# Performance work log

Measured on AMD Instinct MI355X. Metric: run time of the kernel, lower is better.

## Reference

```python
import jax, jax.numpy as jnp
import numpy as np

B, S, D_MODEL, HEADS, DK = 2, 2048, 1024, 16, 64


def setup_inputs() -> dict:
    key = jax.random.key(0)
    ks = jax.random.split(key, 7)
    scale = 0.02
    return {
        "query": jax.random.normal(ks[0], (B, S, D_MODEL), jnp.float32),
        "key": jax.random.normal(ks[1], (B, S, D_MODEL), jnp.float32),
        "value": jax.random.normal(ks[2], (B, S, D_MODEL), jnp.float32),
        "Wq": jax.random.normal(ks[3], (D_MODEL, HEADS * DK), jnp.float32) * scale,
        "bq": jax.random.normal(ks[4], (HEADS * DK,), jnp.float32) * scale,
        "Wo": jax.random.normal(ks[5], (HEADS * DK, D_MODEL), jnp.float32) * scale,
        "bo": jax.random.normal(ks[6], (D_MODEL,), jnp.float32) * scale,
    }


def reference(query, key, value, Wq, bq, Wo, bo):
    # NOTE: faithful to the original code, which (buggily) uses _W_q to
    # project query, key AND value, and scales by sqrt(seq_len), not sqrt(d_k).
    seq_len = key.shape[1]

    def split_heads(x):
        # [B,S,H*DK] -> [H,B,S,DK]; torch chunk(dim=-1)+cat(dim=0) stacks head h
        # (slice h*DK:(h+1)*DK) at batch block h.
        p = x @ Wq + bq
        b, s, _ = p.shape
        return p.reshape(b, s, HEADS, DK).transpose(2, 0, 1, 3)

    q = split_heads(query)   # [H,B,S,DK]
    k = split_heads(key)
    v = split_heads(value)

    inv_scale = jnp.float32(1.0 / np.sqrt(seq_len))
    scores = jnp.einsum("hbqd,hbkd->hbqk", q, k) * inv_scale  # [H,B,S,S]
    attn = jax.nn.softmax(scores, axis=-1)
    out = jnp.einsum("hbqk,hbkd->hbqd", attn, v)  # [H,B,S,DK]
    # inverse of chunk(dim=0)+cat(dim=-1): [H,B,S,DK] -> [B,S,H*DK]
    out = out.transpose(1, 2, 0, 3).reshape(query.shape[0], query.shape[1], HEADS * DK)
    return out @ Wo + bo
```

## Files before the change

kernel.cpp:

```cpp
#include <hip/hip_runtime.h>

#define DEVI __device__ __forceinline__

typedef short short4_t __attribute__((ext_vector_type(4)));
typedef short short8_t __attribute__((ext_vector_type(8)));
typedef __bf16 bf16x8 __attribute__((ext_vector_type(8)));
typedef float f32x4 __attribute__((ext_vector_type(4)));

DEVI short f2bf(float f) {
    union { float f; unsigned u; } v; v.f = f;
    unsigned r = (v.u + 0x7fffu + ((v.u >> 16) & 1u)) >> 16;
    return (short)r;
}

DEVI unsigned pack_ru(float a, float b) {
    union { float f; unsigned u; } x, y; x.f = a; y.f = b;
    return __builtin_amdgcn_perm(y.u + 0x8000u, x.u + 0x8000u, 0x07060302u);
}

DEVI void g2lds16(const short* g, short* l) {
    __builtin_amdgcn_global_load_lds(
        (const __attribute__((address_space(1))) void*)g,
        (__attribute__((address_space(3))) void*)l, 16, 0, 0);
}

__global__ __launch_bounds__(256) void cvt3_kernel(const float* __restrict__ q,
                                                   const float* __restrict__ k,
                                                   const float* __restrict__ v,
                                                   short* __restrict__ X) {
    const size_t N1 = (size_t)4096 * 1024;
    size_t e = ((size_t)blockIdx.x * 256 + threadIdx.x) * 4;
    const float* src; size_t off;
    if (e < N1)            { src = q; off = e; }
    else if (e < 2 * N1)   { src = k; off = e - N1; }
    else                   { src = v; off = e - 2 * N1; }
    f32x4 f = *(const f32x4*)(src + off);
    short4_t o;
    o[0] = f2bf(f[0]); o[1] = f2bf(f[1]); o[2] = f2bf(f[2]); o[3] = f2bf(f[3]);
    *(short4_t*)(X + e) = o;
}

__global__ __launch_bounds__(256) void transpose_w_kernel(const float* __restrict__ W,
                                                          short* __restrict__ Wt) {
    __shared__ short T[64][65];
    const int t = threadIdx.x;
    const int kt = blockIdx.x * 64, nt = blockIdx.y * 64;
#pragma unroll
    for (int r = 0; r < 4; ++r) {
        int kl = (t >> 4) + 16 * r;
        int n0 = (t & 15) * 4;
        f32x4 f = *(const f32x4*)(W + (size_t)(kt + kl) * 1024 + nt + n0);
#pragma unroll
        for (int j = 0; j < 4; ++j) T[n0 + j][kl] = f2bf(f[j]);
    }
    __syncthreads();
#pragma unroll
    for (int r = 0; r < 2; ++r) {
        int nl = (t >> 3) + 32 * r;
        int k0 = (t & 7) * 8;
        short8_t v;
#pragma unroll
        for (int j = 0; j < 8; ++j) v[j] = T[nl][k0 + j];
        *(short8_t*)(Wt + (size_t)(nt + nl) * 1024 + kt + k0) = v;
    }
}

template <typename OutT>
__global__ __launch_bounds__(256) void gemm_bt_kernel(const short* __restrict__ A,
                                                      const short* __restrict__ Bt,
                                                      const float* __restrict__ bias,
                                                      OutT* __restrict__ C,
                                                      int M, int N, int K,
                                                      int qrows, float qscale) {
    __shared__ __align__(16) short As[128 * 32];
    __shared__ __align__(16) short Bs[128 * 32];
    const int tid  = threadIdx.x;
    const int lane = tid & 63, wave = tid >> 6;
    const int quad = lane >> 4, l16 = lane & 15;
    const int row0 = blockIdx.x * 128, col0 = blockIdx.y * 128;
    const int wm = (wave >> 1) * 64, wn = (wave & 1) * 64;
    const int srow = lane >> 2;
    const int scol = (lane & 3) * 8;
    f32x4 acc[4][4] = {};
    for (int k0 = 0; k0 < K; k0 += 32) {
#pragma unroll
        for (int r = 0; r < 2; ++r) {
            int rb = r * 64 + wave * 16;
            g2lds16(A  + (size_t)(row0 + rb + srow) * K + k0 + scol, &As[rb * 32]);
            g2lds16(Bt + (size_t)(col0 + rb + srow) * K + k0 + scol, &Bs[rb * 32]);
        }
        __syncthreads();
        bf16x8 af[4], bfr[4];
#pragma unroll
        for (int mi = 0; mi < 4; ++mi) af[mi]  = *(const bf16x8*)&As[(wm + mi * 16 + l16) * 32 + quad * 8];
#pragma unroll
        for (int ni = 0; ni < 4; ++ni) bfr[ni] = *(const bf16x8*)&Bs[(wn + ni * 16 + l16) * 32 + quad * 8];
#pragma unroll
        for (int mi = 0; mi < 4; ++mi)
#pragma unroll
            for (int ni = 0; ni < 4; ++ni)
                acc[mi][ni] = __builtin_amdgcn_mfma_f32_16x16x32_bf16(af[mi], bfr[ni], acc[mi][ni], 0, 0, 0);
        __syncthreads();
    }
#pragma unroll
    for (int mi = 0; mi < 4; ++mi) {
#pragma unroll
        for (int ni = 0; ni < 4; ++ni) {
            int col = col0 + wn + ni * 16 + l16;
            float bv = bias[col];
#pragma unroll
            for (int i = 0; i < 4; ++i) {
                int row = row0 + wm + mi * 16 + quad * 4 + i;
                float val = acc[mi][ni][i] + bv;
                if (row < qrows) val *= qscale;
                if constexpr (sizeof(OutT) == 2) C[(size_t)row * N + col] = (OutT)f2bf(val);
                else                             C[(size_t)row * N + col] = (OutT)val;
            }
        }
    }
}

__global__ __launch_bounds__(256) void gemm_bt64_kernel(const short* __restrict__ A,
                                                        const short* __restrict__ Bt,
                                                        const float* __restrict__ bias,
                                                        float* __restrict__ C,
                                                        int M, int N, int K) {
    __shared__ __align__(16) short As[64 * 32];
    __shared__ __align__(16) short Bs[128 * 32];
    const int tid  = threadIdx.x;
    const int lane = tid & 63, wave = tid >> 6;
    const int quad = lane >> 4, l16 = lane & 15;
    const int row0 = blockIdx.x * 64, col0 = blockIdx.y * 128;
    const int wn = wave * 32;
    const int srow = lane >> 2;
    const int scol = (lane & 3) * 8;
    f32x4 acc[4][2] = {};
    for (int k0 = 0; k0 < K; k0 += 32) {
        {
            int rb = wave * 16;
            g2lds16(A + (size_t)(row0 + rb + srow) * K + k0 + scol, &As[rb * 32]);
        }
#pragma unroll
        for (int r = 0; r < 2; ++r) {
            int rb = r * 64 + wave * 16;
            g2lds16(Bt + (size_t)(col0 + rb + srow) * K + k0 + scol, &Bs[rb * 32]);
        }
        __syncthreads();
        bf16x8 af[4], bfr[2];
#pragma unroll
        for (int mi = 0; mi < 4; ++mi) af[mi]  = *(const bf16x8*)&As[(mi * 16 + l16) * 32 + quad * 8];
#pragma unroll
        for (int ni = 0; ni < 2; ++ni) bfr[ni] = *(const bf16x8*)&Bs[(wn + ni * 16 + l16) * 32 + quad * 8];
#pragma unroll
        for (int mi = 0; mi < 4; ++mi)
#pragma unroll
            for (int ni = 0; ni < 2; ++ni)
                acc[mi][ni] = __builtin_amdgcn_mfma_f32_16x16x32_bf16(af[mi], bfr[ni], acc[mi][ni], 0, 0, 0);
        __syncthreads();
    }
#pragma unroll
    for (int mi = 0; mi < 4; ++mi) {
#pragma unroll
        for (int ni = 0; ni < 2; ++ni) {
            int col = col0 + wn + ni * 16 + l16;
            float bv = bias[col];
#pragma unroll
            for (int i = 0; i < 4; ++i) {
                int row = row0 + mi * 16 + quad * 4 + i;
                C[(size_t)row * N + col] = acc[mi][ni][i] + bv;
            }
        }
    }
}

__global__ __launch_bounds__(256) void transpose_v_kernel(const short* __restrict__ Pv,
                                                          short* __restrict__ VT) {
    __shared__ short T[64][65];
    const int t = threadIdx.x;
    const int hb = blockIdx.x, st = blockIdx.y * 64;
    const int h = hb >> 1, b = hb & 1;
#pragma unroll
    for (int r = 0; r < 2; ++r) {
        int sl = (t >> 3) + 32 * r;
        short8_t v = *(const short8_t*)(Pv + (size_t)(b * 2048 + st + sl) * 1024 + h * 64 + (t & 7) * 8);
#pragma unroll
        for (int j = 0; j < 8; ++j) T[(t & 7) * 8 + j][sl] = v[j];
    }
    __syncthreads();
#pragma unroll
    for (int r = 0; r < 2; ++r) {
        int dl = (t >> 3) + 32 * r;
        short8_t v;
#pragma unroll
        for (int j = 0; j < 8; ++j) v[j] = T[dl][(t & 7) * 8 + j];
        *(short8_t*)(VT + ((size_t)hb * 64 + dl) * 2048 + st + (t & 7) * 8) = v;
    }
}

__global__ __launch_bounds__(256, 2) void attn_kernel(const short* __restrict__ P,
                                                      const short* __restrict__ VT,
                                                      short* __restrict__ O) {
    constexpr int LDK = 72;
    constexpr int LDV = 136;
    constexpr int LDO = 72;
    union SmemU {
        struct { short Ks[2][128 * LDK]; short Vs[2][64 * LDV]; } s;
        short OT[128 * LDO];
    };
    __shared__ __align__(16) SmemU sm;

    const int t = threadIdx.x;
    const int lane = t & 63, wave = t >> 6;
    const int quad = lane >> 4, l16 = lane & 15;
    const int bx = blockIdx.x;
    const int xcd = bx & 7, bi = bx >> 3;
    const int hb = xcd * 4 + (bi & 3), qt = bi >> 2;
    const int h = hb >> 1, b = hb & 1;
    const short* Pq  = P + (size_t)(b * 2048 + qt * 128) * 1024 + h * 64;
    const short* Pk  = P + (size_t)(4096 + b * 2048) * 1024 + h * 64;
    const short* VTh = VT + (size_t)hb * 64 * 2048;
    const int wq = wave * 32;

    bf16x8 qf[2][2];
#pragma unroll
    for (int miq = 0; miq < 2; ++miq)
#pragma unroll
        for (int kh = 0; kh < 2; ++kh)
            qf[miq][kh] = *(const bf16x8*)(Pq + (size_t)(wq + miq * 16 + l16) * 1024 + kh * 32 + quad * 8);

    bf16x8 ones;
#pragma unroll
    for (int j = 0; j < 8; ++j) ones[j] = (__bf16)1.0f;

    f32x4 oacc[4][2] = {};
    f32x4 osum[2] = {};

    const int krow = t >> 3, kc8 = (t & 7) * 8;
    const int kj = krow & 7, kq = krow >> 3;
    const int lrow32 = (kj >= 4 ? 16 + (kj - 4) : kj) + kq * 4;
    const int vrow = t >> 4, vc8 = (t & 15) * 8;

    short8_t kreg[4], vreg[4];
#pragma unroll
    for (int it = 0; it < 4; ++it) {
        kreg[it] = *(const short8_t*)(Pk + (size_t)(it * 32 + krow) * 1024 + kc8);
        vreg[it] = *(const short8_t*)(VTh + (size_t)(it * 16 + vrow) * 2048 + vc8);
    }

    for (int tile = 0; tile < 16; ++tile) {
        const int buf = tile & 1;
        short* Ksb = sm.s.Ks[buf];
        short* Vsb = sm.s.Vs[buf];
#pragma unroll
        for (int it = 0; it < 4; ++it) {
            *(short8_t*)&Ksb[(it * 32 + lrow32) * LDK + kc8] = kreg[it];
            *(short8_t*)&Vsb[(it * 16 + vrow) * LDV + vc8] = vreg[it];
        }
        __syncthreads();
        if (tile + 1 < 16) {
            int kv0 = (tile + 1) * 128;
#pragma unroll
            for (int it = 0; it < 4; ++it) {
                kreg[it] = *(const short8_t*)(Pk + (size_t)(kv0 + it * 32 + krow) * 1024 + kc8);
                vreg[it] = *(const short8_t*)(VTh + (size_t)(it * 16 + vrow) * 2048 + kv0 + vc8);
            }
        }
#pragma unroll
        for (int p = 0; p < 4; ++p) {
            bf16x8 aA0 = *(const bf16x8*)&Ksb[(p * 32 + l16) * LDK + quad * 8];
            bf16x8 aA1 = *(const bf16x8*)&Ksb[(p * 32 + l16) * LDK + 32 + quad * 8];
            bf16x8 aB0 = *(const bf16x8*)&Ksb[(p * 32 + 16 + l16) * LDK + quad * 8];
            bf16x8 aB1 = *(const bf16x8*)&Ksb[(p * 32 + 16 + l16) * LDK + 32 + quad * 8];
            bf16x8 vA[4];
#pragma unroll
            for (int di = 0; di < 4; ++di)
                vA[di] = *(const bf16x8*)&Vsb[(di * 16 + l16) * LDV + p * 32 + quad * 8];
#pragma unroll
            for (int miq = 0; miq < 2; ++miq) {
                f32x4 sA = {}, sB = {};
                sA = __builtin_amdgcn_mfma_f32_16x16x32_bf16(aA0, qf[miq][0], sA, 0, 0, 0);
                sB = __builtin_amdgcn_mfma_f32_16x16x32_bf16(aB0, qf[miq][0], sB, 0, 0, 0);
                sA = __builtin_amdgcn_mfma_f32_16x16x32_bf16(aA1, qf[miq][1], sA, 0, 0, 0);
                sB = __builtin_amdgcn_mfma_f32_16x16x32_bf16(aB1, qf[miq][1], sB, 0, 0, 0);
                float eA0 = __builtin_amdgcn_exp2f(sA[0]);
                float eA1 = __builtin_amdgcn_exp2f(sA[1]);
                float eA2 = __builtin_amdgcn_exp2f(sA[2]);
                float eA3 = __builtin_amdgcn_exp2f(sA[3]);
                float eB0 = __builtin_amdgcn_exp2f(sB[0]);
                float eB1 = __builtin_amdgcn_exp2f(sB[1]);
                float eB2 = __builtin_amdgcn_exp2f(sB[2]);
                float eB3 = __builtin_amdgcn_exp2f(sB[3]);
                union { unsigned u[4]; bf16x8 b8; } pb;
                pb.u[0] = pack_ru(eA0, eA1);
                pb.u[1] = pack_ru(eA2, eA3);
                pb.u[2] = pack_ru(eB0, eB1);
                pb.u[3] = pack_ru(eB2, eB3);
                osum[miq] = __builtin_amdgcn_mfma_f32_16x16x32_bf16(ones, pb.b8, osum[miq], 0, 0, 0);
#pragma unroll
                for (int di = 0; di < 4; ++di)
                    oacc[di][miq] = __builtin_amdgcn_mfma_f32_16x16x32_bf16(vA[di], pb.b8, oacc[di][miq], 0, 0, 0);
            }
        }
    }

    float rinv[2];
#pragma unroll
    for (int miq = 0; miq < 2; ++miq) rinv[miq] = 1.0f / osum[miq][0];

    __syncthreads();

#pragma unroll
    for (int di = 0; di < 4; ++di) {
#pragma unroll
        for (int miq = 0; miq < 2; ++miq) {
            float v0 = oacc[di][miq][0] * rinv[miq];
            float v1 = oacc[di][miq][1] * rinv[miq];
            float v2 = oacc[di][miq][2] * rinv[miq];
            float v3 = oacc[di][miq][3] * rinv[miq];
            uint2 w;
            w.x = pack_ru(v0, v1);
            w.y = pack_ru(v2, v3);
            int q = wq + miq * 16 + l16;
            *(uint2*)&sm.OT[q * LDO + di * 16 + quad * 4] = w;
        }
    }
    __syncthreads();
    {
        const int orow = t >> 1, ocol = (t & 1) * 32;
        short* dst = O + (size_t)(b * 2048 + qt * 128 + orow) * 1024 + h * 64 + ocol;
#pragma unroll
        for (int c = 0; c < 4; ++c)
            *(short8_t*)(dst + c * 8) = *(const short8_t*)&sm.OT[orow * LDO + ocol + c * 8];
    }
}

extern "C" void kernel_launch(void* const* d_in, const int* in_sizes, int n_in,
                              void* d_out, int out_size, void* d_ws, size_t ws_size,
                              hipStream_t stream) {
    (void)in_sizes; (void)n_in; (void)out_size; (void)ws_size;
    const float* q  = (const float*)d_in[0];
    const float* k  = (const float*)d_in[1];
    const float* v  = (const float*)d_in[2];
    const float* Wq = (const float*)d_in[3];
    const float* bq = (const float*)d_in[4];
    const float* Wo = (const float*)d_in[5];
    const float* bo = (const float*)d_in[6];
    float* out = (float*)d_out;

    short* Xcat = (short*)d_ws;
    short* WqT  = Xcat + (size_t)12288 * 1024;
    short* WoT  = WqT + (size_t)1024 * 1024;
    short* P    = WoT + (size_t)1024 * 1024;
    short* VT   = P + (size_t)12288 * 1024;
    short* O    = VT + (size_t)32 * 64 * 2048;

    const float qscale = 0.022097086912079608f * 1.4426950408889634f;

    cvt3_kernel<<<12288, 256, 0, stream>>>(q, k, v, Xcat);
    transpose_w_kernel<<<dim3(16, 16), 256, 0, stream>>>(Wq, WqT);
    transpose_w_kernel<<<dim3(16, 16), 256, 0, stream>>>(Wo, WoT);
    gemm_bt_kernel<short><<<dim3(96, 8), 256, 0, stream>>>(Xcat, WqT, bq, P, 12288, 1024, 1024, 4096, qscale);
    transpose_v_kernel<<<dim3(32, 32), 256, 0, stream>>>(P + (size_t)8192 * 1024, VT);
    attn_kernel<<<512, 256, 0, stream>>>(P, VT, O);
    gemm_bt64_kernel<<<dim3(64, 8), 256, 0, stream>>>(O, WoT, bo, out, 4096, 1024, 1024);
}
```

Measured before the change: 214.6 us.

## Double-buffer GEMM LDS tiles, merge prep kernels, raise attention MFMA priority

Merges the fp32-to-bf16 input conversion and both weight transposes into a single prep launch, removing two kernel launches. Both GEMM kernels now keep two LDS buffers and issue the next K-tile's global-to-LDS loads before computing on the current one, dropping one barrier per iteration so load latency can overlap MFMA work. The attention inner loop wraps its MFMA/exp section in s_setprio to favour that wave in scheduling. Double buffering doubles LDS use per block, which can lower occupancy. The prefetch relies on the single remaining barrier per iteration to order the async LDS writes against reads.

Result: faster. 205.6 us (-4.2%).

```diff
diff --git a/kernel.cpp b/kernel.cpp
--- a/kernel.cpp
+++ b/kernel.cpp
@@ -24,27 +24,35 @@
         (__attribute__((address_space(3))) void*)l, 16, 0, 0);
 }
 
-__global__ __launch_bounds__(256) void cvt3_kernel(const float* __restrict__ q,
+__global__ __launch_bounds__(256) void prep_kernel(const float* __restrict__ q,
                                                    const float* __restrict__ k,
                                                    const float* __restrict__ v,
-                                                   short* __restrict__ X) {
-    const size_t N1 = (size_t)4096 * 1024;
-    size_t e = ((size_t)blockIdx.x * 256 + threadIdx.x) * 4;
-    const float* src; size_t off;
-    if (e < N1)            { src = q; off = e; }
-    else if (e < 2 * N1)   { src = k; off = e - N1; }
-    else                   { src = v; off = e - 2 * N1; }
-    f32x4 f = *(const f32x4*)(src + off);
-    short4_t o;
-    o[0] = f2bf(f[0]); o[1] = f2bf(f[1]); o[2] = f2bf(f[2]); o[3] = f2bf(f[3]);
-    *(short4_t*)(X + e) = o;
-}
-
-__global__ __launch_bounds__(256) void transpose_w_kernel(const float* __restrict__ W,
-                                                          short* __restrict__ Wt) {
+                                                   short* __restrict__ X,
+                                                   const float* __restrict__ Wq,
+                                                   short* __restrict__ WqT,
+                                                   const float* __restrict__ Wo,
+                                                   short* __restrict__ WoT) {
     __shared__ short T[64][65];
+    const int bx = blockIdx.x;
     const int t = threadIdx.x;
-    const int kt = blockIdx.x * 64, nt = blockIdx.y * 64;
+    if (bx < 12288) {
+        const size_t N1 = (size_t)4096 * 1024;
+        size_t e = ((size_t)bx * 256 + t) * 4;
+        const float* src; size_t off;
+        if (e < N1)            { src = q; off = e; }
+        else if (e < 2 * N1)   { src = k; off = e - N1; }
+        else                   { src = v; off = e - 2 * N1; }
+        f32x4 f = *(const f32x4*)(src + off);
+        short4_t o;
+        o[0] = f2bf(f[0]); o[1] = f2bf(f[1]); o[2] = f2bf(f[2]); o[3] = f2bf(f[3]);
+        *(short4_t*)(X + e) = o;
+        return;
+    }
+    const int which = bx - 12288;
+    const float* W = (which < 256) ? Wq : Wo;
+    short* Wt      = (which < 256) ? WqT : WoT;
+    const int bxx = which & 255;
+    const int kt = (bxx & 15) * 64, nt = (bxx >> 4) * 64;
 #pragma unroll
     for (int r = 0; r < 4; ++r) {
         int kl = (t >> 4) + 16 * r;
@@ -58,10 +66,10 @@
     for (int r = 0; r < 2; ++r) {
         int nl = (t >> 3) + 32 * r;
         int k0 = (t & 7) * 8;
-        short8_t v;
-#pragma unroll
-        for (int j = 0; j < 8; ++j) v[j] = T[nl][k0 + j];
-        *(short8_t*)(Wt + (size_t)(nt + nl) * 1024 + kt + k0) = v;
+        short8_t vv;
+#pragma unroll
+        for (int j = 0; j < 8; ++j) vv[j] = T[nl][k0 + j];
+        *(short8_t*)(Wt + (size_t)(nt + nl) * 1024 + kt + k0) = vv;
     }
 }
 
@@ -72,8 +80,8 @@
                                                       OutT* __restrict__ C,
                                                       int M, int N, int K,
                                                       int qrows, float qscale) {
-    __shared__ __align__(16) short As[128 * 32];
-    __shared__ __align__(16) short Bs[128 * 32];
+    __shared__ __align__(16) short As[2][128 * 32];
+    __shared__ __align__(16) short Bs[2][128 * 32];
     const int tid  = threadIdx.x;
     const int lane = tid & 63, wave = tid >> 6;
     const int quad = lane >> 4, l16 = lane & 15;
@@ -82,25 +90,35 @@
     const int srow = lane >> 2;
     const int scol = (lane & 3) * 8;
     f32x4 acc[4][4] = {};
+#pragma unroll
+    for (int r = 0; r < 2; ++r) {
+        int rb = r * 64 + wave * 16;
+        g2lds16(A  + (size_t)(row0 + rb + srow) * K + scol, &As[0][rb * 32]);
+        g2lds16(Bt + (size_t)(col0 + rb + srow) * K + scol, &Bs[0][rb * 32]);
+    }
+    __syncthreads();
+    int buf = 0;
     for (int k0 = 0; k0 < K; k0 += 32) {
-#pragma unroll
-        for (int r = 0; r < 2; ++r) {
-            int rb = r * 64 + wave * 16;
-            g2lds16(A  + (size_t)(row0 + rb + srow) * K + k0 + scol, &As[rb * 32]);
-            g2lds16(Bt + (size_t)(col0 + rb + srow) * K + k0 + scol, &Bs[rb * 32]);
-        }
-        __syncthreads();
+        if (k0 + 32 < K) {
+#pragma unroll
+            for (int r = 0; r < 2; ++r) {
+                int rb = r * 64 + wave * 16;
+                g2lds16(A  + (size_t)(row0 + rb + srow) * K + k0 + 32 + scol, &As[buf ^ 1][rb * 32]);
+                g2lds16(Bt + (size_t)(col0 + rb + srow) * K + k0 + 32 + scol, &Bs[buf ^ 1][rb * 32]);
+            }
+        }
         bf16x8 af[4], bfr[4];
 #pragma unroll
-        for (int mi = 0; mi < 4; ++mi) af[mi]  = *(const bf16x8*)&As[(wm + mi * 16 + l16) * 32 + quad * 8];
-#pragma unroll
-        for (int ni = 0; ni < 4; ++ni) bfr[ni] = *(const bf16x8*)&Bs[(wn + ni * 16 + l16) * 32 + quad * 8];
+        for (int mi = 0; mi < 4; ++mi) af[mi]  = *(const bf16x8*)&As[buf][(wm + mi * 16 + l16) * 32 + quad * 8];
+#pragma unroll
+        for (int ni = 0; ni < 4; ++ni) bfr[ni] = *(const bf16x8*)&Bs[buf][(wn + ni * 16 + l16) * 32 + quad * 8];
 #pragma unroll
         for (int mi = 0; mi < 4; ++mi)
 #pragma unroll
             for (int ni = 0; ni < 4; ++ni)
                 acc[mi][ni] = __builtin_amdgcn_mfma_f32_16x16x32_bf16(af[mi], bfr[ni], acc[mi][ni], 0, 0, 0);
         __syncthreads();
+        buf ^= 1;
     }
 #pragma unroll
     for (int mi = 0; mi < 4; ++mi) {
@@ -125,8 +143,8 @@
                                                         const float* __restrict__ bias,
                                                         float* __restrict__ C,
                                                         int M, int N, int K) {
-    __shared__ __align__(16) short As[64 * 32];
-    __shared__ __align__(16) short Bs[128 * 32];
+    __shared__ __align__(16) short As[2][64 * 32];
+    __shared__ __align__(16) short Bs[2][128 * 32];
     const int tid  = threadIdx.x;
     const int lane = tid & 63, wave = tid >> 6;
     const int quad = lane >> 4, l16 = lane & 15;
@@ -135,28 +153,39 @@
     const int srow = lane >> 2;
     const int scol = (lane & 3) * 8;
     f32x4 acc[4][2] = {};
+    {
+        int rb = wave * 16;
+        g2lds16(A + (size_t)(row0 + rb + srow) * K + scol, &As[0][rb * 32]);
+#pragma unroll
+        for (int r = 0; r < 2; ++r) {
+            int rb2 = r * 64 + wave * 16;
+            g2lds16(Bt + (size_t)(col0 + rb2 + srow) * K + scol, &Bs[0][rb2 * 32]);
+        }
+    }
+    __syncthreads();
+    int buf = 0;
     for (int k0 = 0; k0 < K; k0 += 32) {
-        {
+        if (k0 + 32 < K) {
             int rb = wave * 16;
-            g2lds16(A + (size_t)(row0 + rb + srow) * K + k0 + scol, &As[rb * 32]);
-        }
-#pragma unroll
-        for (int r = 0; r < 2; ++r) {
-            int rb = r * 64 + wave * 16;
-            g2lds16(Bt + (size_t)(col0 + rb + srow) * K + k0 + scol, &Bs[rb * 32]);
-        }
-        __syncthreads();
+            g2lds16(A + (size_t)(row0 + rb + srow) * K + k0 + 32 + scol, &As[buf ^ 1][rb * 32]);
+#pragma unroll
+            for (int r = 0; r < 2; ++r) {
+                int rb2 = r * 64 + wave * 16;
+                g2lds16(Bt + (size_t)(col0 + rb2 + srow) * K + k0 + 32 + scol, &Bs[buf ^ 1][rb2 * 32]);
+            }
+        }
         bf16x8 af[4], bfr[2];
 #pragma unroll
-        for (int mi = 0; mi < 4; ++mi) af[mi]  = *(const bf16x8*)&As[(mi * 16 + l16) * 32 + quad * 8];
-#pragma unroll
-        for (int ni = 0; ni < 2; ++ni) bfr[ni] = *(const bf16x8*)&Bs[(wn + ni * 16 + l16) * 32 + quad * 8];
+        for (int mi = 0; mi < 4; ++mi) af[mi]  = *(const bf16x8*)&As[buf][(mi * 16 + l16) * 32 + quad * 8];
+#pragma unroll
+        for (int ni = 0; ni < 2; ++ni) bfr[ni] = *(const bf16x8*)&Bs[buf][(wn + ni * 16 + l16) * 32 + quad * 8];
 #pragma unroll
         for (int mi = 0; mi < 4; ++mi)
 #pragma unroll
             for (int ni = 0; ni < 2; ++ni)
                 acc[mi][ni] = __builtin_amdgcn_mfma_f32_16x16x32_bf16(af[mi], bfr[ni], acc[mi][ni], 0, 0, 0);
         __syncthreads();
+        buf ^= 1;
     }
 #pragma unroll
     for (int mi = 0; mi < 4; ++mi) {
@@ -275,6 +304,7 @@
 #pragma unroll
             for (int di = 0; di < 4; ++di)
                 vA[di] = *(const bf16x8*)&Vsb[(di * 16 + l16) * LDV + p * 32 + quad * 8];
+            __builtin_amdgcn_s_setprio(1);
 #pragma unroll
             for (int miq = 0; miq < 2; ++miq) {
                 f32x4 sA = {}, sB = {};
@@ -300,6 +330,7 @@
                 for (int di = 0; di < 4; ++di)
                     oacc[di][miq] = __builtin_amdgcn_mfma_f32_16x16x32_bf16(vA[di], pb.b8, oacc[di][miq], 0, 0, 0);
             }
+            __builtin_amdgcn_s_setprio(0);
         }
     }
 
@@ -356,9 +387,7 @@
 
     const float qscale = 0.022097086912079608f * 1.4426950408889634f;
 
-    cvt3_kernel<<<12288, 256, 0, stream>>>(q, k, v, Xcat);
-    transpose_w_kernel<<<dim3(16, 16), 256, 0, stream>>>(Wq, WqT);
-    transpose_w_kernel<<<dim3(16, 16), 256, 0, stream>>>(Wo, WoT);
+    prep_kernel<<<12800, 256, 0, stream>>>(q, k, v, Xcat, Wq, WqT, Wo, WoT);
     gemm_bt_kernel<short><<<dim3(96, 8), 256, 0, stream>>>(Xcat, WqT, bq, P, 12288, 1024, 1024, 4096, qscale);
     transpose_v_kernel<<<dim3(32, 32), 256, 0, stream>>>(P + (size_t)8192 * 1024, VT);
     attn_kernel<<<512, 256, 0, stream>>>(P, VT, O);
```
